# Kernel tuning notes

Measured on AMD Instinct MI355X. Metric: run time of the kernel, lower is better.

The kernel has to match this reference:

```python
import jax, jax.numpy as jnp
import numpy as np

OUT_FEATURES = 4096
IN_FEATURES = 4096
GROUP_SIZE = 128
NUM_GROUPS = OUT_FEATURES // GROUP_SIZE  # groups along output-channel axis (axis=0)


def _unpack_int8_to_int4(packed, num_elements):
    # Each int8 byte holds two signed int4 values: low nibble first, then high nibble.
    p = packed.astype(jnp.int8)
    low = jnp.right_shift(jnp.left_shift(p, 4), 4)   # sign-extended low nibble, in [-8, 7]
    high = jnp.right_shift(p, 4)                      # arithmetic shift -> sign-extended high nibble
    vals = jnp.stack([low, high], axis=-1).reshape(-1)
    return vals[:num_elements]


def _dequantize_weight(packed_weight, scales, zero_points):
    int4 = _unpack_int8_to_int4(packed_weight, OUT_FEATURES * IN_FEATURES)
    w = int4.astype(jnp.float32).reshape(NUM_GROUPS, GROUP_SIZE, IN_FEATURES)
    # per-group (over output channels): (q - zp) * scale
    w = (w - zero_points[:, None, None]) * scales[:, None, None]
    return w.reshape(OUT_FEATURES, IN_FEATURES)


def setup_inputs() -> dict:
    key = jax.random.key(0)
    k_x, k_w, k_s, k_zp, k_b = jax.random.split(key, 5)
    x = jax.random.normal(k_x, (8192, IN_FEATURES), dtype=jnp.float32)
    # packed int4 weights stored as signed bytes
    packed_weight = jax.random.randint(k_w, (OUT_FEATURES * IN_FEATURES // 2,), 0, 256, dtype=jnp.int32) - 128
    scales = jax.random.uniform(k_s, (NUM_GROUPS,), dtype=jnp.float32) * 0.02 + 0.001
    zero_points = jax.random.normal(k_zp, (NUM_GROUPS,), dtype=jnp.float32) * 0.5
    bias = jax.random.normal(k_b, (OUT_FEATURES,), dtype=jnp.float32)
    return {"x": x, "packed_weight": packed_weight, "scales": scales,
            "zero_points": zero_points, "bias": bias}


def reference(x, packed_weight, scales, zero_points, bias):
    weight = _dequantize_weight(packed_weight, scales, zero_points)  # [out, in]
    return jnp.einsum('bi,oi->bo', x, weight) + bias
```

## Files before the change

kernel.cpp:

```cpp
#include <hip/hip_runtime.h>
#include <cstdint>
#include <cstddef>

#define M_DIM 8192
#define N_DIM 4096
#define K_DIM 4096
#define CHUNK_M 4096

typedef __attribute__((ext_vector_type(8))) short bf16x8;
typedef __attribute__((ext_vector_type(4))) float floatx4;

__device__ __forceinline__ ushort f2bf_rne(float f) {
    union { float f; uint32_t u; } a;
    a.f = f;
    uint32_t u = a.u;
    uint32_t r = (u + 0x7fffu + ((u >> 16) & 1u)) >> 16;
    return (ushort)r;
}

__device__ __forceinline__ uint32_t pk_bf_trunc(float f0, float f1) {
    return __builtin_amdgcn_perm(__float_as_uint(f1), __float_as_uint(f0),
                                 0x07060302u);
}

__global__ void dequant_w_kernel(const int4* __restrict__ pw,
                                 const float* __restrict__ scales,
                                 const float* __restrict__ zps,
                                 uint4* __restrict__ wb, int np4) {
    int p4 = blockIdx.x * blockDim.x + threadIdx.x;
    if (p4 >= np4) return;
    int p = p4 * 4;
    int g = p >> 18;
    float s = scales[g];
    float b = -zps[g] * s;
    int4 v = pw[p4];
    int vv[4] = { v.x, v.y, v.z, v.w };
    ushort o[8];
#pragma unroll
    for (int j = 0; j < 4; ++j) {
        int lo = ((int)((uint32_t)vv[j] << 28)) >> 28;
        int hi = ((int)((uint32_t)vv[j] << 24)) >> 28;
        o[2 * j]     = f2bf_rne(fmaf((float)lo, s, b));
        o[2 * j + 1] = f2bf_rne(fmaf((float)hi, s, b));
    }
    uint4 st;
    st.x = (uint32_t)o[0] | ((uint32_t)o[1] << 16);
    st.y = (uint32_t)o[2] | ((uint32_t)o[3] << 16);
    st.z = (uint32_t)o[4] | ((uint32_t)o[5] << 16);
    st.w = (uint32_t)o[6] | ((uint32_t)o[7] << 16);
    wb[p4] = st;
}

__global__ void convert_x_kernel(const float4* __restrict__ x4,
                                 ushort4* __restrict__ out4, int n4) {
    int i = blockIdx.x * blockDim.x + threadIdx.x;
    if (i >= n4) return;
    float4 v = x4[i];
    ushort4 o;
    o.x = f2bf_rne(v.x);
    o.y = f2bf_rne(v.y);
    o.z = f2bf_rne(v.z);
    o.w = f2bf_rne(v.w);
    out4[i] = o;
}

#define TBM 256
#define TBN 256
#define TBK 32
#define NT  (K_DIM / TBK)
#define A_E 8192
#define SLOT_E 16384

__global__ __launch_bounds__(512, 2)
void gemm_bf16_256(const ushort* __restrict__ A,
                   const ushort* __restrict__ B,
                   const float* __restrict__ bias,
                   float* __restrict__ C) {
    __shared__ ushort lds[4 * SLOT_E];

    const int tid  = threadIdx.x;
    const int lane = tid & 63;
    const int wave = tid >> 6;
    const int wm   = wave >> 2;
    const int wn   = wave & 3;

    const int nwg = gridDim.x;
    const int cpx = nwg >> 3;
    const int bid = blockIdx.x;
    const int swz = (bid & 7) * cpx + (bid >> 3);
    const int bn  = swz & (N_DIM / TBN - 1);
    const int bm  = swz / (N_DIM / TBN);

    const ushort* Ab = A + (size_t)(bm * TBM) * K_DIM;
    const ushort* Bb = B + (size_t)(bn * TBN) * K_DIM;

    const int srow = tid >> 2;
    const int scol = (((tid & 3) ^ ((tid >> 3) & 3)) * 8);
    const ushort* gA0 = Ab + (size_t)srow * K_DIM + scol;
    const ushort* gA1 = gA0 + (size_t)128 * K_DIM;
    const ushort* gB0 = Bb + (size_t)srow * K_DIM + scol;
    const ushort* gB1 = gB0 + (size_t)128 * K_DIM;
    const int wdst = wave * 512;

    const int frow = lane & 15;
    const int fcol = (((lane >> 4) ^ ((frow >> 1) & 3)) * 8);
    const int aoff = (wm * 128 + frow) * TBK + fcol;
    const int boff = A_E + (wn * 64 + frow) * TBK + fcol;

    floatx4 acc[8][4] = {};

#define STAGE_A(tt)                                                           \
    {                                                                          \
        const int k0s = ((tt) & (NT - 1)) * TBK;                               \
        ushort* d = lds + ((tt) & 3) * SLOT_E + wdst;                          \
        __builtin_amdgcn_global_load_lds(                                      \
            (const __attribute__((address_space(1))) void*)(gA0 + k0s),        \
            (__attribute__((address_space(3))) void*)d, 16, 0, 0);             \
        __builtin_amdgcn_global_load_lds(                                      \
            (const __attribute__((address_space(1))) void*)(gA1 + k0s),        \
            (__attribute__((address_space(3))) void*)(d + 4096), 16, 0, 0);    \
    }
#define STAGE_B(tt)                                                           \
    {                                                                          \
        const int k0s = ((tt) & (NT - 1)) * TBK;                               \
        ushort* d = lds + ((tt) & 3) * SLOT_E + A_E + wdst;                    \
        __builtin_amdgcn_global_load_lds(                                      \
            (const __attribute__((address_space(1))) void*)(gB0 + k0s),        \
            (__attribute__((address_space(3))) void*)d, 16, 0, 0);             \
        __builtin_amdgcn_global_load_lds(                                      \
            (const __attribute__((address_space(1))) void*)(gB1 + k0s),        \
            (__attribute__((address_space(3))) void*)(d + 4096), 16, 0, 0);    \
    }

#define BODY(T, afc, bfc, afn, bfn)                                           \
    {                                                                          \
        const ushort* bcur = lds + ((T) & 3) * SLOT_E;                         \
        const ushort* bnxt = lds + (((T) + 1) & 3) * SLOT_E;                   \
        bf16x8 afb[4];                                                         \
             \
             \
        _Pragma("unroll")                                                      \
        for (int i = 0; i < 4; ++i)                                            \
            afb[i] = *(const bf16x8*)(bcur + aoff + (4 + i) * 512);            \
        _Pragma("unroll")                                                      \
        for (int j = 0; j < 4; ++j)                                            \
            bfn[j] = *(const bf16x8*)(bnxt + boff + j * 512);                  \
        _Pragma("unroll")                                                      \
        for (int i = 0; i < 4; ++i)                                            \
            afn[i] = *(const bf16x8*)(bnxt + aoff + i * 512);                  \
        STAGE_A((T) + 3) STAGE_B((T) + 3)                                      \
        __builtin_amdgcn_sched_barrier(0);                                     \
        __builtin_amdgcn_s_setprio(1);                                         \
        _Pragma("unroll")                                                      \
        for (int i = 0; i < 4; ++i)                                            \
            _Pragma("unroll")                                                  \
            for (int j = 0; j < 4; ++j)                                        \
                acc[i][j] = __builtin_amdgcn_mfma_f32_16x16x32_bf16(           \
                    afc[i], bfc[j], acc[i][j], 0, 0, 0);                       \
        _Pragma("unroll")                                                      \
        for (int i = 0; i < 4; ++i)                                            \
            _Pragma("unroll")                                                  \
            for (int j = 0; j < 4; ++j)                                        \
                acc[4 + i][j] = __builtin_amdgcn_mfma_f32_16x16x32_bf16(       \
                    afb[i], bfc[j], acc[4 + i][j], 0, 0, 0);                   \
        __builtin_amdgcn_s_setprio(0);                                         \
        asm volatile("s_waitcnt vmcnt(4)" ::: "memory");                       \
        __builtin_amdgcn_s_barrier();                                          \
        __builtin_amdgcn_sched_barrier(0);                                     \
    }

    STAGE_A(0) STAGE_B(0)
    STAGE_A(1) STAGE_B(1)
    STAGE_A(2) STAGE_B(2)
    asm volatile("s_waitcnt vmcnt(4)" ::: "memory");
    __builtin_amdgcn_s_barrier();
    __builtin_amdgcn_sched_barrier(0);

    bf16x8 af0[4], bf0[4], af1[4], bf1[4];
#pragma unroll
    for (int j = 0; j < 4; ++j)
        bf0[j] = *(const bf16x8*)(lds + boff + j * 512);
#pragma unroll
    for (int i = 0; i < 4; ++i)
        af0[i] = *(const bf16x8*)(lds + aoff + i * 512);

    for (int t = 0; t < NT; t += 2) {
        BODY(t,     af0, bf0, af1, bf1)
        BODY(t + 1, af1, bf1, af0, bf0)
    }
#undef BODY
#undef STAGE_A
#undef STAGE_B

    const int crow0 = bm * TBM + wm * 128;
    const int ccol0 = bn * TBN + wn * 64;
    const int rl = lane >> 4;
    const int cl = lane & 15;
#pragma unroll
    for (int j = 0; j < 4; ++j) {
        const int col = ccol0 + j * 16 + cl;
        const float bv = bias[col];
#pragma unroll
        for (int i = 0; i < 8; ++i) {
            const int row = crow0 + i * 16 + rl * 4;
            float* cp = C + (size_t)row * N_DIM + col;
#pragma unroll
            for (int r = 0; r < 4; ++r)
                cp[(size_t)r * N_DIM] = acc[i][j][r] + bv;
        }
    }
}

#define BM 128
#define BN 128
#define BK 32

__global__ void gemm_fused_kernel(const float* __restrict__ X,
                                  const ushort* __restrict__ B,
                                  const float* __restrict__ bias,
                                  float* __restrict__ C) {
    __shared__ ushort As[BM * BK];
    __shared__ ushort Bs[BN * BK];

    const int tid  = threadIdx.x;
    const int lane = tid & 63;
    const int wave = tid >> 6;
    const int wm   = wave >> 1;
    const int wn   = wave & 1;
    const int bm   = blockIdx.y;
    const int bn   = blockIdx.x;

    const int ar = tid >> 2;
    const int ac = (tid & 3) * 8;
    const float* xp0 = X + (size_t)(bm * BM + ar) * K_DIM + ac;
    const float* xp1 = xp0 + (size_t)64 * K_DIM;
    ushort* as0 = As + ar * BK + ac;
    ushort* as1 = as0 + 64 * BK;

    const int scol = (lane & 3) * 8;
    const ushort* Bb = B + (size_t)(bn * BN) * K_DIM;

    floatx4 acc[4][4] = {};

    for (int k0 = 0; k0 < K_DIM; k0 += BK) {
        float4 a0 = *(const float4*)(xp0 + k0);
        float4 a1 = *(const float4*)(xp0 + k0 + 4);
        float4 b0 = *(const float4*)(xp1 + k0);
        float4 b1 = *(const float4*)(xp1 + k0 + 4);
#pragma unroll
        for (int q = 0; q < 2; ++q) {
            const int chunk = wave * 2 + q;
            const int r = chunk * 16 + (lane >> 2);
            const ushort* gb = Bb + (size_t)r * K_DIM + k0 + scol;
            __builtin_amdgcn_global_load_lds(
                (const __attribute__((address_space(1))) void*)gb,
                (__attribute__((address_space(3))) void*)(Bs + chunk * 512),
                16, 0, 0);
        }
        uint4 w0, w1;
        w0.x = pk_bf_trunc(a0.x, a0.y);
        w0.y = pk_bf_trunc(a0.z, a0.w);
        w0.z = pk_bf_trunc(a1.x, a1.y);
        w0.w = pk_bf_trunc(a1.z, a1.w);
        w1.x = pk_bf_trunc(b0.x, b0.y);
        w1.y = pk_bf_trunc(b0.z, b0.w);
        w1.z = pk_bf_trunc(b1.x, b1.y);
        w1.w = pk_bf_trunc(b1.z, b1.w);
        *(uint4*)as0 = w0;
        *(uint4*)as1 = w1;

        __syncthreads();

        bf16x8 af[4], bfr[4];
        const int frow = lane & 15;
        const int fcol = (lane >> 4) * 8;
#pragma unroll
        for (int i = 0; i < 4; ++i) {
            af[i]  = *(const bf16x8*)(As + (wm * 64 + i * 16 + frow) * BK + fcol);
            bfr[i] = *(const bf16x8*)(Bs + (wn * 64 + i * 16 + frow) * BK + fcol);
        }
#pragma unroll
        for (int i = 0; i < 4; ++i)
#pragma unroll
            for (int j = 0; j < 4; ++j)
                acc[i][j] = __builtin_amdgcn_mfma_f32_16x16x32_bf16(
                    af[i], bfr[j], acc[i][j], 0, 0, 0);
        __syncthreads();
    }

    const int crow0 = bm * BM + wm * 64;
    const int ccol0 = bn * BN + wn * 64;
    const int rl = lane >> 4;
    const int cl = lane & 15;
#pragma unroll
    for (int j = 0; j < 4; ++j) {
        const int col = ccol0 + j * 16 + cl;
        const float bv = bias[col];
#pragma unroll
        for (int i = 0; i < 4; ++i) {
            const int row = crow0 + i * 16 + rl * 4;
            float* cp = C + (size_t)row * N_DIM + col;
#pragma unroll
            for (int r = 0; r < 4; ++r)
                cp[(size_t)r * N_DIM] = acc[i][j][r] + bv;
        }
    }
}

extern "C" void kernel_launch(void* const* d_in, const int* in_sizes, int n_in,
                              void* d_out, int out_size, void* d_ws, size_t ws_size,
                              hipStream_t stream) {
    const float* x      = (const float*)d_in[0];
    const int*   pw     = (const int*)d_in[1];
    const float* scales = (const float*)d_in[2];
    const float* zps    = (const float*)d_in[3];
    const float* bias   = (const float*)d_in[4];
    float* out = (float*)d_out;

    ushort* wb = (ushort*)d_ws;

    {
        int np4 = (N_DIM * K_DIM / 2) / 4;
        dequant_w_kernel<<<np4 / 256, 256, 0, stream>>>(
            (const int4*)pw, scales, zps, (uint4*)wb, np4);
    }

    const size_t need_full  = ((size_t)N_DIM * K_DIM + (size_t)M_DIM * K_DIM) * 2;
    const size_t need_chunk = ((size_t)N_DIM * K_DIM + (size_t)CHUNK_M * K_DIM) * 2;

    if (ws_size >= need_full) {
        ushort* xb = wb + (size_t)N_DIM * K_DIM;
        int n4 = (M_DIM * K_DIM) / 4;
        convert_x_kernel<<<n4 / 256, 256, 0, stream>>>(
            (const float4*)x, (ushort4*)xb, n4);
        int nblk = (M_DIM / TBM) * (N_DIM / TBN);
        gemm_bf16_256<<<nblk, 512, 0, stream>>>(xb, wb, bias, out);
    } else if (ws_size >= need_chunk) {
        ushort* xb = wb + (size_t)N_DIM * K_DIM;
        for (int c = 0; c < M_DIM / CHUNK_M; ++c) {
            const float* xc = x + (size_t)c * CHUNK_M * K_DIM;
            float* oc = out + (size_t)c * CHUNK_M * N_DIM;
            int n4 = (CHUNK_M * K_DIM) / 4;
            convert_x_kernel<<<n4 / 256, 256, 0, stream>>>(
                (const float4*)xc, (ushort4*)xb, n4);
            int nblk = (CHUNK_M / TBM) * (N_DIM / TBN);
            gemm_bf16_256<<<nblk, 512, 0, stream>>>(xb, wb, bias, oc);
        }
    } else {
        dim3 grid(N_DIM / BN, M_DIM / BM);
        gemm_fused_kernel<<<grid, 256, 0, stream>>>(x, wb, bias, out);
    }
}
```

Measured before the change: 472.0 us.

## Interleave LDS fragment loads and global-to-LDS staging between MFMA sub-blocks

The main loop body used to issue every LDS fragment read and both global-to-LDS stages for the next tile in one burst, then run all 32 MFMAs. Now the MFMA block is split into four quarters, and the A staging, the B fragment reads plus B staging, and the A fragment reads are placed between them, with sched_barriers and an explicit lgkmcnt wait. The aim is to keep memory-instruction issue from stalling the matrix cores and to hide LDS latency behind compute. In exchange there are more scheduling barriers and priority toggles, and the hand-picked waitcnt could be too tight or too loose.

```diff
diff --git a/kernel.cpp b/kernel.cpp
--- a/kernel.cpp
+++ b/kernel.cpp
@@ -137,28 +137,56 @@
         const ushort* bcur = lds + ((T) & 3) * SLOT_E;                         \
         const ushort* bnxt = lds + (((T) + 1) & 3) * SLOT_E;                   \
         bf16x8 afb[4];                                                         \
-             \
-             \
+                                             \
         _Pragma("unroll")                                                      \
         for (int i = 0; i < 4; ++i)                                            \
             afb[i] = *(const bf16x8*)(bcur + aoff + (4 + i) * 512);            \
-        _Pragma("unroll")                                                      \
-        for (int j = 0; j < 4; ++j)                                            \
-            bfn[j] = *(const bf16x8*)(bnxt + boff + j * 512);                  \
-        _Pragma("unroll")                                                      \
-        for (int i = 0; i < 4; ++i)                                            \
-            afn[i] = *(const bf16x8*)(bnxt + aoff + i * 512);                  \
-        STAGE_A((T) + 3) STAGE_B((T) + 3)                                      \
+        STAGE_A((T) + 3)                                                       \
         __builtin_amdgcn_sched_barrier(0);                                     \
         __builtin_amdgcn_s_setprio(1);                                         \
         _Pragma("unroll")                                                      \
-        for (int i = 0; i < 4; ++i)                                            \
+        for (int i = 0; i < 2; ++i)                                            \
             _Pragma("unroll")                                                  \
             for (int j = 0; j < 4; ++j)                                        \
                 acc[i][j] = __builtin_amdgcn_mfma_f32_16x16x32_bf16(           \
                     afc[i], bfc[j], acc[i][j], 0, 0, 0);                       \
+        __builtin_amdgcn_s_setprio(0);                                         \
+        __builtin_amdgcn_sched_barrier(0);                                     \
+                                             \
+        _Pragma("unroll")                                                      \
+        for (int j = 0; j < 4; ++j)                                            \
+            bfn[j] = *(const bf16x8*)(bnxt + boff + j * 512);                  \
+        STAGE_B((T) + 3)                                                       \
+        __builtin_amdgcn_sched_barrier(0);                                     \
+        __builtin_amdgcn_s_setprio(1);                                         \
+        _Pragma("unroll")                                                      \
+        for (int i = 2; i < 4; ++i)                                            \
+            _Pragma("unroll")                                                  \
+            for (int j = 0; j < 4; ++j)                                        \
+                acc[i][j] = __builtin_amdgcn_mfma_f32_16x16x32_bf16(           \
+                    afc[i], bfc[j], acc[i][j], 0, 0, 0);                       \
+        __builtin_amdgcn_s_setprio(0);                                         \
+        __builtin_amdgcn_sched_barrier(0);                                     \
+                                                            \
         _Pragma("unroll")                                                      \
         for (int i = 0; i < 4; ++i)                                            \
+            afn[i] = *(const bf16x8*)(bnxt + aoff + i * 512);                  \
+        __builtin_amdgcn_sched_barrier(0);                                     \
+                \
+        asm volatile("s_waitcnt lgkmcnt(8)" ::: "memory");                     \
+        __builtin_amdgcn_sched_barrier(0);                                     \
+        __builtin_amdgcn_s_setprio(1);                                         \
+        _Pragma("unroll")                                                      \
+        for (int i = 0; i < 2; ++i)                                            \
+            _Pragma("unroll")                                                  \
+            for (int j = 0; j < 4; ++j)                                        \
+                acc[4 + i][j] = __builtin_amdgcn_mfma_f32_16x16x32_bf16(       \
+                    afb[i], bfc[j], acc[4 + i][j], 0, 0, 0);                   \
+        __builtin_amdgcn_s_setprio(0);                                         \
+        __builtin_amdgcn_sched_barrier(0);                                     \
+        __builtin_amdgcn_s_setprio(1);                                         \
+        _Pragma("unroll")                                                      \
+        for (int i = 2; i < 4; ++i)                                            \
             _Pragma("unroll")                                                  \
             for (int j = 0; j < 4; ++j)                                        \
                 acc[4 + i][j] = __builtin_amdgcn_mfma_f32_16x16x32_bf16(       \
```

Result: no change. 464.3 us (-1.6%).
